# Kernel tuning notes

Measured on AMD Instinct MI355X. Metric: run time of the kernel, lower is better.

## Reference

```python
import jax, jax.numpy as jnp
import numpy as np

N = 4096      # num utterances (graph nodes)
D = 512       # utt_embed_size * 2
W = 10        # att_window_size
S = 8         # num speakers
WIN = 2 * W + 1


def setup_inputs() -> dict:
    key = jax.random.key(0)
    ks = jax.random.split(key, 7)
    s = 0.05  # keep activations in a sane range through two layers
    return {
        "context_embeds": jax.random.normal(ks[0], (N, D), jnp.float32),
        "speakers": jax.random.randint(ks[1], (N,), 0, S),
        "w_gc1": jax.random.normal(ks[2], (4, D, D), jnp.float32) * s,
        "w_gc2": jax.random.normal(ks[3], (4, D, D), jnp.float32) * s,
        "w_att": jax.random.normal(ks[4], (D, D), jnp.float32) * s,
        "w_aggr1": jax.random.normal(ks[5], (D, D), jnp.float32) * s,
        "w_aggr2": jax.random.normal(ks[6], (D, D), jnp.float32) * s,
    }


def _relation_adjs(x, speakers, w_att):
    """Windowed edge attention + 4 relation-masked adjacency matrices."""
    n = x.shape[0]
    pad = jnp.zeros((W, D), x.dtype)
    padded = jnp.concatenate([pad, x, pad], axis=0)          # [n+2W, D]
    # banded gather: row j sees padded[j : j+2W+1]  == cols j-W .. j+W
    gidx = jnp.arange(n)[:, None] + jnp.arange(WIN)[None, :]
    fat = padded[gidx]
    raw = jnp.einsum('nwd,ed->nwe', fat, w_att)               # Linear: x @ W^T
    scores = jnp.einsum('nwe,ne->nw', raw, x)
    attn = jax.nn.softmax(scores, axis=1)                     # softmax over full window (pads included, as original)
    # scatter attention into a banded [n, n] mask
    cols = jnp.arange(n)[:, None] + jnp.arange(WIN)[None, :] - W
    valid = (cols >= 0) & (cols < n)
    rows = jnp.broadcast_to(jnp.arange(n)[:, None], cols.shape)
    attn_mask = jnp.zeros((n, n), x.dtype).at[
        rows, jnp.clip(cols, 0, n - 1)].add(jnp.where(valid, attn, 0.0))
    i = jnp.arange(n)[:, None]
    j = jnp.arange(n)[None, :]
    band = jnp.abs(j - i) <= W
    same_spk = speakers[:, None] == speakers[None, :]
    pred = ((j >= i) & band).astype(x.dtype) * attn_mask      # successors-in-time kept (triu) within window
    suc = ((j < i) & band).astype(x.dtype) * attn_mask        # strict past within window
    same = (same_spk & band).astype(x.dtype) * attn_mask
    diff = ((~same_spk) & band).astype(x.dtype) * attn_mask
    return jnp.stack([pred, suc, same, diff])                 # [4, n, n]


def _gcn_layer(h, adjs, w_gc, w_aggr):
    # sum_r  A_r @ (h @ W_r)  + h @ W_aggr, then relu
    hw = jnp.einsum('md,rde->rme', h, w_gc)                   # [4, n, D]
    agg = jnp.einsum('rnm,rme->ne', adjs, hw)                 # [n, D]
    return jax.nn.relu(agg + h @ w_aggr)


def reference(context_embeds, speakers, w_gc1, w_gc2, w_att, w_aggr1, w_aggr2):
    adjs = _relation_adjs(context_embeds, speakers, w_att)
    h1 = _gcn_layer(context_embeds, adjs, w_gc1, w_aggr1)
    h2 = _gcn_layer(h1, adjs, w_gc2, w_aggr2)
    return h2
```

## Files before the change

kernel.cpp:

```cpp
#include <hip/hip_runtime.h>


#define NN 4096

typedef __bf16 bf16x8 __attribute__((ext_vector_type(8)));
typedef float f32x4 __attribute__((ext_vector_type(4)));
typedef unsigned short u16;
typedef unsigned int u32;

__device__ __forceinline__ u16 f2bf(float f) {
  unsigned u = __float_as_uint(f);
  unsigned r = u + 0x7FFFu + ((u >> 16) & 1u);
  return (u16)(r >> 16);
}
__device__ __forceinline__ float bf2f(u16 h) {
  return __uint_as_float(((unsigned)h) << 16);
}
__device__ __forceinline__ float blo(u32 v) { return __uint_as_float(v << 16); }
__device__ __forceinline__ float bhi(u32 v) { return __uint_as_float(v & 0xffff0000u); }
__device__ __forceinline__ u32 packbf(float a, float b) {
  return (u32)f2bf(a) | ((u32)f2bf(b) << 16);
}

__device__ __forceinline__ void gload_lds16(const u16* g, u16* l) {
  __builtin_amdgcn_global_load_lds(
      (const __attribute__((address_space(1))) void*)g,
      (__attribute__((address_space(3))) void*)l, 16, 0, 0);
}

__global__ void prep_all(const float* __restrict__ x, const float* __restrict__ w_att,
                         const float* __restrict__ w_gc1, const float* __restrict__ w_aggr1,
                         const float* __restrict__ w_gc2, const float* __restrict__ w_aggr2,
                         const int* __restrict__ spk,
                         u16* __restrict__ Aatt, u16* __restrict__ Batt,
                         u16* __restrict__ Wt1, u16* __restrict__ Wt2,
                         float* __restrict__ xp, u32* __restrict__ xWg,
                         u32* __restrict__ h1Wg, int* __restrict__ spkp) {
  const int b = blockIdx.x, tid = threadIdx.x;
  if (b < 8192) {
    int idx = b * 256 + tid;
    int r = idx >> 9, c = idx & 511;
    float v = x[idx];
    u16 hi = f2bf(v), lo = f2bf(v - bf2f(hi));
    u16* row = Aatt + (size_t)r * 1536;
    row[c] = hi; row[512 + c] = lo; row[1024 + c] = hi;
    xp[(size_t)(r + 16) * 512 + c] = v;
  } else if (b < 9216) {
    int idx = (b - 8192) * 256 + tid;
    int j = idx >> 9, e = idx & 511;
    float v = w_att[(size_t)e * 512 + j];
    u16 hi = f2bf(v), lo = f2bf(v - bf2f(hi));
    u16* row = Batt + (size_t)j * 1536;
    row[e] = hi; row[512 + e] = hi; row[1024 + e] = lo;
  } else if (b < 17408) {
    int lay = (b >= 13312);
    int idx = (b - (lay ? 13312 : 9216)) * 256 + tid;
    const float* g = lay ? w_gc2 : w_gc1;
    const float* wa = lay ? w_aggr2 : w_aggr1;
    u16* Wt = lay ? Wt2 : Wt1;
    int j = idx >> 9, k = idx & 511;
    int p = j >> 9, jj = j & 511;
    size_t o = (size_t)k * 512 + jj;
    float v;
    if (p == 0)      v = g[o] - g[262144 + o];
    else if (p == 1) v = g[524288 + o] - g[786432 + o];
    else if (p == 2) v = g[262144 + o] + g[786432 + o];
    else             v = wa[o];
    Wt[(size_t)j * 512 + k] = f2bf(v);
  } else if (b < 17472) {
    int idx = (b - 17408) * 256 + tid;
    int g = idx >> 9, c = idx & 511;
    int row = (g < 16) ? g : 4112 + (g - 16);
    xp[(size_t)row * 512 + c] = 0.f;
  } else if (b < 17600) {
    int idx = (b - 17472) * 256 + tid;
    int g = idx >> 10, c = idx & 1023;
    int row = (g < 16) ? g : 4112 + (g - 16);
    xWg[(size_t)row * 1024 + c] = 0;
  } else if (b < 17728) {
    int idx = (b - 17600) * 256 + tid;
    int g = idx >> 10, c = idx & 1023;
    int row = (g < 16) ? g : 4112 + (g - 16);
    h1Wg[(size_t)row * 1024 + c] = 0;
  } else {
    int idx = (b - 17728) * 256 + tid;
    if (idx < 4128)
      spkp[idx] = (idx >= 16 && idx < 4112) ? spk[idx - 16] : -9;
  }
}

__device__ __forceinline__ void xcd_swz(int gx, int& bx, int& by) {
  int lid = by * gx + bx;
  int cpx = (gx * (int)gridDim.y) >> 3;
  int nl = (lid & 7) * cpx + (lid >> 3);
  by = nl / gx;
  bx = nl - by * gx;
}

__device__ __forceinline__ void gemm_core(const u16* __restrict__ A, const u16* __restrict__ Bt,
                                          int K, int lda, int ldb, size_t bm, size_t bn,
                                          u16 (&As)[2][8192], u16 (&Bs)[2][8192],
                                          f32x4 (&acc)[4][4]) {
  const int tid = threadIdx.x;
  const int lane = tid & 63;
  const int wave = tid >> 6;
  const int wr = wave >> 1, wc = wave & 1;
  const int arow = wr * 64 + (lane & 15);
  const int bcol = wc * 64 + (lane & 15);
  const int nt = K >> 6;

  auto STAGE = [&](int t, int bi) {
    const int k0 = t << 6;
#pragma unroll
    for (int c4 = 0; c4 < 4; ++c4) {
      const int o = (c4 * 256 + tid) * 16;
      const int r = o >> 7;
      const int sc = (((o >> 4) & 7) ^ (r & 7)) << 3;
      gload_lds16(A + (bm + r) * lda + k0 + sc, &As[bi][o >> 1]);
      gload_lds16(Bt + (bn + r) * ldb + k0 + sc, &Bs[bi][o >> 1]);
    }
  };

  STAGE(0, 0);
  for (int t = 0; t < nt; ++t) {
    const int cur = t & 1;
    if (t + 1 < nt) {
      STAGE(t + 1, cur ^ 1);
      asm volatile("s_waitcnt vmcnt(8)" ::: "memory");
    } else {
      asm volatile("s_waitcnt vmcnt(0)" ::: "memory");
    }
    __builtin_amdgcn_s_barrier();
    asm volatile("" ::: "memory");
    bf16x8 af[4][2], bfr[4][2];
#pragma unroll
    for (int i = 0; i < 4; ++i)
#pragma unroll
      for (int ks = 0; ks < 2; ++ks) {
        const int ar = arow + i * 16;
        const int ac = ((ks * 4 + (lane >> 4)) ^ (ar & 7)) << 4;
        af[i][ks] = *(const bf16x8*)((const char*)&As[cur][0] + ar * 128 + ac);
        const int br = bcol + i * 16;
        const int bc = ((ks * 4 + (lane >> 4)) ^ (br & 7)) << 4;
        bfr[i][ks] = *(const bf16x8*)((const char*)&Bs[cur][0] + br * 128 + bc);
      }
#pragma unroll
    for (int ks = 0; ks < 2; ++ks)
#pragma unroll
      for (int i = 0; i < 4; ++i)
#pragma unroll
        for (int j = 0; j < 4; ++j)
          acc[i][j] = __builtin_amdgcn_mfma_f32_16x16x32_bf16(af[i][ks], bfr[j][ks],
                                                              acc[i][j], 0, 0, 0);
    asm volatile("s_waitcnt lgkmcnt(0)" ::: "memory");
    __builtin_amdgcn_sched_barrier(0);
    __builtin_amdgcn_s_barrier();
  }
}

__global__ __launch_bounds__(256, 2) void fat_gemm(const u16* __restrict__ Aatt,
                                                   const u16* __restrict__ Wt1,
                                                   const u16* __restrict__ Batt,
                                                   u16* __restrict__ xW, float* __restrict__ y) {
  __shared__ u16 As[2][8192];
  __shared__ u16 Bs[2][8192];
  f32x4 acc[4][4] = {};
  const int tid = threadIdx.x;
  const int lane = tid & 63;
  const int wave = tid >> 6;
  const int wr = wave >> 1, wc = wave & 1;
  int bx = blockIdx.x, by = blockIdx.y;
  xcd_swz(20, bx, by);
  const size_t bm = (size_t)by * 128;
  const bool yp = bx < 4;
  const size_t bn = yp ? (size_t)bx * 128 : (size_t)(bx - 4) * 128;

  if (yp)
    gemm_core(Aatt, Batt, 1536, 1536, 1536, bm, bn, As, Bs, acc);
  else
    gemm_core(Aatt, Wt1, 512, 1536, 512, bm, bn, As, Bs, acc);

  const size_t crow = bm + wr * 64 + ((lane >> 4) * 4);
  const size_t ccol = bn + wc * 64 + (lane & 15);
#pragma unroll
  for (int i = 0; i < 4; ++i)
#pragma unroll
    for (int j = 0; j < 4; ++j)
#pragma unroll
      for (int b = 0; b < 4; ++b) {
        size_t r = crow + i * 16 + b, c = ccol + j * 16;
        if (yp)
          y[r * 512 + c] = acc[i][j][b];
        else
          xW[r * 2048 + c] = f2bf(acc[i][j][b]);
      }
}

__global__ __launch_bounds__(256, 2) void gemm_l2(const u16* __restrict__ h1,
                                                  const u16* __restrict__ Wt2,
                                                  u16* __restrict__ h1W) {
  __shared__ u16 As[2][8192];
  __shared__ u16 Bs[2][8192];
  f32x4 acc[4][4] = {};
  const int tid = threadIdx.x;
  const int lane = tid & 63;
  const int wave = tid >> 6;
  const int wr = wave >> 1, wc = wave & 1;
  int bx = blockIdx.x, by = blockIdx.y;
  xcd_swz(16, bx, by);
  const size_t bm = (size_t)by * 128;
  const size_t bn = (size_t)bx * 128;
  gemm_core(h1, Wt2, 512, 512, 512, bm, bn, As, Bs, acc);
  const size_t crow = bm + wr * 64 + ((lane >> 4) * 4);
  const size_t ccol = bn + wc * 64 + (lane & 15);
#pragma unroll
  for (int i = 0; i < 4; ++i)
#pragma unroll
    for (int j = 0; j < 4; ++j)
#pragma unroll
      for (int b = 0; b < 4; ++b) {
        size_t r = crow + i * 16 + b, c = ccol + j * 16;
        h1W[r * 2048 + c] = f2bf(acc[i][j][b]);
      }
}

template <int PH>
__global__ __launch_bounds__(256, 2) void bandagg(const u32* __restrict__ P32,
                                                  const float* __restrict__ xp,
                                                  const float* __restrict__ y,
                                                  float* __restrict__ attn,
                                                  const int* __restrict__ spkp,
                                                  void* __restrict__ out) {
  const int b = blockIdx.x;
  const int n0 = (((b & 7) << 6) + (b >> 3)) << 3;
  const int tid = threadIdx.x;
  __shared__ float at[8][24];
  __shared__ int spb[28];
  __shared__ float ys[8][512];

  if (tid < 28) spb[tid] = spkp[16 + n0 - 10 + tid];
  if (PH == 1) {
    for (int i = tid; i < 4096; i += 256)
      ys[i >> 9][i & 511] = y[(size_t)(n0 + (i >> 9)) * 512 + (i & 511)];
  } else {
    if (tid < 192) at[tid / 24][tid % 24] = attn[(size_t)(n0 + tid / 24) * 24 + tid % 24];
  }
  __syncthreads();

  if (PH == 1) {
    const int wv = tid >> 6, lane = tid & 63;
    for (int rr = wv; rr < 8; rr += 4) {
      const int n = n0 + rr;
      for (int w = 0; w < 21; ++w) {
        const float* xm = xp + (size_t)(n + 6 + w) * 512;
        float p = 0.f;
#pragma unroll
        for (int i = 0; i < 8; ++i) p += xm[lane + i * 64] * ys[rr][lane + i * 64];
#pragma unroll
        for (int off = 32; off; off >>= 1) p += __shfl_xor(p, off, 64);
        if (lane == 0) at[rr][w] = p;
      }
      float v = (lane < 21) ? at[rr][lane] : -1e30f;
      float mx = v;
#pragma unroll
      for (int off = 32; off; off >>= 1) mx = fmaxf(mx, __shfl_xor(mx, off, 64));
      float e = (lane < 21) ? __expf(v - mx) : 0.f;
      float sum = e;
#pragma unroll
      for (int off = 32; off; off >>= 1) sum += __shfl_xor(sum, off, 64);
      if (lane < 21) {
        int m = n + lane - 10;
        float a = (0 <= m && m < NN) ? (e / sum) : 0.f;
        at[rr][lane] = a;
        attn[(size_t)n * 24 + lane] = a;
      }
    }
    __syncthreads();
  }

  const int c = tid;
  u32 vP[28], vS[28], vA[28];
#pragma unroll
  for (int j = 0; j < 28; ++j) {
    const u32* rowp = P32 + (ptrdiff_t)(n0 - 10 + j) * 1024 + c;
    vP[j] = rowp[0];
    vS[j] = rowp[256];
    vA[j] = rowp[512];
  }
  int sb[28];
#pragma unroll
  for (int j = 0; j < 28; ++j) sb[j] = spb[j];

#pragma unroll
  for (int r = 0; r < 8; ++r) {
    float wv_[21];
#pragma unroll
    for (int w = 0; w < 21; ++w) wv_[w] = at[r][w];
    const int s0 = sb[10 + r];
    u32 sv = P32[(size_t)(n0 + r) * 1024 + 768 + c];
    float aL = blo(sv), aH = bhi(sv);
#pragma unroll
    for (int w = 0; w < 21; ++w) {
      const int j = r + w;
      const float a = wv_[w];
      const float as = (sb[j] == s0) ? a : 0.f;
      aL += a * blo(vA[j]) + as * blo(vS[j]);
      aH += a * bhi(vA[j]) + as * bhi(vS[j]);
      if (w >= 10) {
        aL += a * blo(vP[j]);
        aH += a * bhi(vP[j]);
      }
    }
    aL = fmaxf(aL, 0.f);
    aH = fmaxf(aH, 0.f);
    if (PH == 1) {
      ((u32*)out)[(size_t)(n0 + r) * 256 + c] = packbf(aL, aH);
    } else {
      float2 o = {aL, aH};
      ((float2*)out)[(size_t)(n0 + r) * 256 + c] = o;
    }
  }
}

extern "C" void kernel_launch(void* const* d_in, const int* in_sizes, int n_in,
                              void* d_out, int out_size, void* d_ws, size_t ws_size,
                              hipStream_t stream) {
  const float* x = (const float*)d_in[0];
  const int* spk = (const int*)d_in[1];
  const float* w_gc1 = (const float*)d_in[2];
  const float* w_gc2 = (const float*)d_in[3];
  const float* w_att = (const float*)d_in[4];
  const float* w_aggr1 = (const float*)d_in[5];
  const float* w_aggr2 = (const float*)d_in[6];

  char* p = (char*)d_ws;
  u16* Aatt = (u16*)p;  p += (size_t)NN * 1536 * 2;
  u16* Batt = (u16*)p;  p += (size_t)512 * 1536 * 2;
  u16* Wt1 = (u16*)p;   p += (size_t)2048 * 512 * 2;
  u16* Wt2 = (u16*)p;   p += (size_t)2048 * 512 * 2;
  float* xp = (float*)p; p += (size_t)4128 * 512 * 4;
  float* y = (float*)p; p += (size_t)NN * 512 * 4;
  float* attn = (float*)p; p += (size_t)NN * 24 * 4;
  u16* xWg = (u16*)p;   p += (size_t)4128 * 2048 * 2;
  u16* h1 = (u16*)p;    p += (size_t)NN * 512 * 2;
  u16* h1Wg = (u16*)p;  p += (size_t)4128 * 2048 * 2;
  int* spkp = (int*)p;  p += (size_t)4128 * 4;

  u16* xW = xWg + (size_t)16 * 2048;
  u16* h1W = h1Wg + (size_t)16 * 2048;

  prep_all<<<17745, 256, 0, stream>>>(x, w_att, w_gc1, w_aggr1, w_gc2, w_aggr2, spk,
                                      Aatt, Batt, Wt1, Wt2, xp, (u32*)xWg, (u32*)h1Wg,
                                      spkp);

  fat_gemm<<<dim3(20, 32), 256, 0, stream>>>(Aatt, Wt1, Batt, xW, y);

  bandagg<1><<<512, 256, 0, stream>>>((const u32*)xW, xp, y, attn, spkp, h1);

  gemm_l2<<<dim3(16, 32), 256, 0, stream>>>(h1, Wt2, h1W);

  bandagg<2><<<512, 256, 0, stream>>>((const u32*)h1W, xp, y, attn, spkp, d_out);
}
```

Before: 106.2 us.

## Split banded aggregation into 2-row blocks with parallel score dot products

Replaces the 8-rows-per-block band aggregation kernel with a 2-rows-per-block kernel launched on four times as many blocks. The 42 attention dot products are spread across all four wavefronts instead of looping per row, and speaker-masked weights are precomputed in shared memory. This aims to raise parallelism and occupancy and cut register pressure. The cost is more redundant loads of neighbouring rows, 22 rows per 2 outputs instead of 28 per 8.

```diff
diff --git a/kernel.cpp b/kernel.cpp
--- a/kernel.cpp
+++ b/kernel.cpp
@@ -224,43 +224,48 @@
       }
 }
 
+__device__ __forceinline__ int xcd_pair(int b) {
+  return ((((b & 7) << 8) + (b >> 3)) << 1);
+}
+
 template <int PH>
-__global__ __launch_bounds__(256, 2) void bandagg(const u32* __restrict__ P32,
-                                                  const float* __restrict__ xp,
-                                                  const float* __restrict__ y,
-                                                  float* __restrict__ attn,
-                                                  const int* __restrict__ spkp,
-                                                  void* __restrict__ out) {
-  const int b = blockIdx.x;
-  const int n0 = (((b & 7) << 6) + (b >> 3)) << 3;
+__global__ __launch_bounds__(256) void gather2r(const u32* __restrict__ P32,
+                                                const float* __restrict__ xp,
+                                                const float* __restrict__ y,
+                                                float* __restrict__ attn,
+                                                const int* __restrict__ spkp,
+                                                void* __restrict__ out) {
+  const int n0 = xcd_pair(blockIdx.x);
   const int tid = threadIdx.x;
-  __shared__ float at[8][24];
-  __shared__ int spb[28];
-  __shared__ float ys[8][512];
-
-  if (tid < 28) spb[tid] = spkp[16 + n0 - 10 + tid];
+  __shared__ float ys[2][512];
+  __shared__ float sc[2][21];
+  __shared__ float avs[2][21], asvs[2][21];
+  __shared__ int sps[22];
+
+  if (tid < 22) sps[tid] = spkp[16 + n0 - 10 + tid];
+  __syncthreads();
+
   if (PH == 1) {
-    for (int i = tid; i < 4096; i += 256)
+    for (int i = tid; i < 1024; i += 256)
       ys[i >> 9][i & 511] = y[(size_t)(n0 + (i >> 9)) * 512 + (i & 511)];
-  } else {
-    if (tid < 192) at[tid / 24][tid % 24] = attn[(size_t)(n0 + tid / 24) * 24 + tid % 24];
-  }
-  __syncthreads();
-
-  if (PH == 1) {
+    __syncthreads();
     const int wv = tid >> 6, lane = tid & 63;
-    for (int rr = wv; rr < 8; rr += 4) {
+    for (int pidx = wv; pidx < 42; pidx += 4) {
+      const int rr = (pidx >= 21) ? 1 : 0;
+      const int w = pidx - (rr ? 21 : 0);
+      const float* xm = xp + (size_t)(n0 + rr + 6 + w) * 512;
+      float p = 0.f;
+#pragma unroll
+      for (int i = 0; i < 8; ++i) p += xm[lane + i * 64] * ys[rr][lane + i * 64];
+#pragma unroll
+      for (int off = 32; off; off >>= 1) p += __shfl_xor(p, off, 64);
+      if (lane == 0) sc[rr][w] = p;
+    }
+    __syncthreads();
+    if (tid < 128) {
+      const int rr = tid >> 6, lane = tid & 63;
       const int n = n0 + rr;
-      for (int w = 0; w < 21; ++w) {
-        const float* xm = xp + (size_t)(n + 6 + w) * 512;
-        float p = 0.f;
-#pragma unroll
-        for (int i = 0; i < 8; ++i) p += xm[lane + i * 64] * ys[rr][lane + i * 64];
-#pragma unroll
-        for (int off = 32; off; off >>= 1) p += __shfl_xor(p, off, 64);
-        if (lane == 0) at[rr][w] = p;
-      }
-      float v = (lane < 21) ? at[rr][lane] : -1e30f;
+      float v = (lane < 21) ? sc[rr][lane] : -1e30f;
       float mx = v;
 #pragma unroll
       for (int off = 32; off; off >>= 1) mx = fmaxf(mx, __shfl_xor(mx, off, 64));
@@ -271,54 +276,62 @@
       if (lane < 21) {
         int m = n + lane - 10;
         float a = (0 <= m && m < NN) ? (e / sum) : 0.f;
-        at[rr][lane] = a;
+        avs[rr][lane] = a;
+        asvs[rr][lane] = (sps[lane + rr] == spkp[16 + n]) ? a : 0.f;
         attn[(size_t)n * 24 + lane] = a;
       }
     }
     __syncthreads();
-  }
-
-  const int c = tid;
-  u32 vP[28], vS[28], vA[28];
-#pragma unroll
-  for (int j = 0; j < 28; ++j) {
-    const u32* rowp = P32 + (ptrdiff_t)(n0 - 10 + j) * 1024 + c;
-    vP[j] = rowp[0];
-    vS[j] = rowp[256];
-    vA[j] = rowp[512];
-  }
-  int sb[28];
-#pragma unroll
-  for (int j = 0; j < 28; ++j) sb[j] = spb[j];
-
-#pragma unroll
-  for (int r = 0; r < 8; ++r) {
-    float wv_[21];
-#pragma unroll
-    for (int w = 0; w < 21; ++w) wv_[w] = at[r][w];
-    const int s0 = sb[10 + r];
-    u32 sv = P32[(size_t)(n0 + r) * 1024 + 768 + c];
-    float aL = blo(sv), aH = bhi(sv);
-#pragma unroll
-    for (int w = 0; w < 21; ++w) {
-      const int j = r + w;
-      const float a = wv_[w];
-      const float as = (sb[j] == s0) ? a : 0.f;
-      aL += a * blo(vA[j]) + as * blo(vS[j]);
-      aH += a * bhi(vA[j]) + as * bhi(vS[j]);
-      if (w >= 10) {
-        aL += a * blo(vP[j]);
-        aH += a * bhi(vP[j]);
-      }
-    }
-    aL = fmaxf(aL, 0.f);
-    aH = fmaxf(aH, 0.f);
-    if (PH == 1) {
-      ((u32*)out)[(size_t)(n0 + r) * 256 + c] = packbf(aL, aH);
-    } else {
-      float2 o = {aL, aH};
-      ((float2*)out)[(size_t)(n0 + r) * 256 + c] = o;
-    }
+  } else {
+    if (tid < 128) {
+      const int rr = tid >> 6, lane = tid & 63;
+      const int n = n0 + rr;
+      if (lane < 21) {
+        float a = attn[(size_t)n * 24 + lane];
+        avs[rr][lane] = a;
+        asvs[rr][lane] = (sps[lane + rr] == spkp[16 + n]) ? a : 0.f;
+      }
+    }
+    __syncthreads();
+  }
+
+  u32 s0 = P32[(size_t)n0 * 1024 + 768 + tid];
+  u32 s1 = P32[(size_t)(n0 + 1) * 1024 + 768 + tid];
+  float a0L = blo(s0), a0H = bhi(s0);
+  float a1L = blo(s1), a1H = bhi(s1);
+#pragma unroll
+  for (int j = 0; j < 22; ++j) {
+    const u32* row = P32 + (ptrdiff_t)(n0 - 10 + j) * 1024 + tid;
+    const u32 va = row[512], vs = row[256];
+    const float al = blo(va), ah = bhi(va), sl = blo(vs), sh = bhi(vs);
+    float pl = 0.f, ph = 0.f;
+    if (j >= 10) {
+      const u32 vp = row[0];
+      pl = blo(vp);
+      ph = bhi(vp);
+    }
+    if (j < 21) {
+      const float a = avs[0][j], as = asvs[0][j];
+      a0L += a * al + as * sl;
+      a0H += a * ah + as * sh;
+      if (j >= 10) { a0L += a * pl; a0H += a * ph; }
+    }
+    if (j >= 1) {
+      const float a = avs[1][j - 1], as = asvs[1][j - 1];
+      a1L += a * al + as * sl;
+      a1H += a * ah + as * sh;
+      if (j >= 11) { a1L += a * pl; a1H += a * ph; }
+    }
+  }
+  a0L = fmaxf(a0L, 0.f); a0H = fmaxf(a0H, 0.f);
+  a1L = fmaxf(a1L, 0.f); a1H = fmaxf(a1H, 0.f);
+  if (PH == 1) {
+    ((u32*)out)[(size_t)n0 * 256 + tid] = packbf(a0L, a0H);
+    ((u32*)out)[(size_t)(n0 + 1) * 256 + tid] = packbf(a1L, a1H);
+  } else {
+    float2 v0 = {a0L, a0H}, v1 = {a1L, a1H};
+    ((float2*)out)[(size_t)n0 * 256 + tid] = v0;
+    ((float2*)out)[(size_t)(n0 + 1) * 256 + tid] = v1;
   }
 }
 
@@ -355,9 +368,9 @@
 
   fat_gemm<<<dim3(20, 32), 256, 0, stream>>>(Aatt, Wt1, Batt, xW, y);
 
-  bandagg<1><<<512, 256, 0, stream>>>((const u32*)xW, xp, y, attn, spkp, h1);
+  gather2r<1><<<2048, 256, 0, stream>>>((const u32*)xW, xp, y, attn, spkp, h1);
 
   gemm_l2<<<dim3(16, 32), 256, 0, stream>>>(h1, Wt2, h1W);
 
-  bandagg<2><<<512, 256, 0, stream>>>((const u32*)h1W, xp, y, attn, spkp, d_out);
-}
+  gather2r<2><<<2048, 256, 0, stream>>>((const u32*)h1W, xp, y, attn, spkp, d_out);
+}
```

Measured after the change: 102.9 us. 1.03x faster.
